# Kernel optimization log

Hardware: AMD Instinct MI355X
Metric: run time of the kernel (lower is better)

The kernel has to match this reference:

```python
import jax, jax.numpy as jnp
import numpy as np

B, T, F, OUT = 32, 8192, 128, 1024

def setup_inputs() -> dict:
    key = jax.random.key(0)
    kx, kl = jax.random.split(key)
    x = jax.random.normal(kx, (B, T, F), dtype=jnp.float32)
    # true (unpadded) lengths; module assumes max(lengths) == T (padded length)
    lengths = jax.random.randint(kl, (B,), OUT + 1, T + 1)
    lengths = lengths.at[0].set(T)
    return {"x": x, "lengths": lengths, "output_size": OUT}

def reference(x, lengths, output_size):
    # Original math: per-sample box filter of length f_b = lengths_b - output_size + 1
    # (ones / f_b, zero-padded to max) applied as grouped conv over time:
    #   out[b, t, f] = (1/f_b) * sum_{k=0}^{f_b-1} x[b, t+k, f],  t in [0, output_size)
    # Implemented via prefix sums instead of materializing the sparse filter bank.
    fsize = lengths - output_size + 1                                  # [B]
    cs = jnp.cumsum(x, axis=1)                                         # [B, T, F]
    cs = jnp.concatenate([jnp.zeros_like(cs[:, :1]), cs], axis=1)      # [B, T+1, F]
    t = jnp.arange(output_size)                                        # [OUT]
    idx = (t[None, :] + fsize[:, None])[:, :, None]                    # [B, OUT, 1]
    hi = jnp.take_along_axis(cs, idx, axis=1)                          # [B, OUT, F]
    lo = cs[:, :output_size, :]                                        # [B, OUT, F]
    return (hi - lo) / fsize[:, None, None].astype(x.dtype)
```

## Files before the change

### kernel.cpp

```cpp
#include <hip/hip_runtime.h>

#define NB   32
#define NT   8192
#define NF   128
#define NOUT 1024
#define SEGSZ 128
#define NSEG  64
#define NCHUNK 8

__device__ __forceinline__ float4 f4add(float4 a, float4 b) {
  return make_float4(a.x + b.x, a.y + b.y, a.z + b.z, a.w + b.w);
}
__device__ __forceinline__ float4 f4sub(float4 a, float4 b) {
  return make_float4(a.x - b.x, a.y - b.y, a.z - b.z, a.w - b.w);
}

__global__ __launch_bounds__(256) void seg_sums(const float* __restrict__ x,
                                                const int* __restrict__ lengths,
                                                float* __restrict__ S) {
  const int blk = blockIdx.x;
  const int b   = blk >> 6;
  const int seg = blk & (NSEG - 1);
  const int len = lengths[b];
  if (seg * SEGSZ >= len) return;

  const int tid = threadIdx.x;
  const int f4  = tid & 31;
  const int tl  = tid >> 5;

  const float4* xp =
      reinterpret_cast<const float4*>(x + (size_t)b * NT * NF +
                                      (size_t)(seg * SEGSZ) * NF) + f4;
  float4 acc = make_float4(0.f, 0.f, 0.f, 0.f);
  #pragma unroll 4
  for (int r = tl; r < SEGSZ; r += 8)
    acc = f4add(acc, xp[r * 32]);

  __shared__ float4 red[8][32];
  red[tl][f4] = acc;
  __syncthreads();
  if (tl == 0) {
    float4 s = red[0][f4];
    #pragma unroll
    for (int k = 1; k < 8; ++k) s = f4add(s, red[k][f4]);
    reinterpret_cast<float4*>(S + ((size_t)b * NSEG + seg) * NF)[f4] = s;
  }
}

__global__ __launch_bounds__(256) void window_avg(const float* __restrict__ x,
                                                  const int* __restrict__ lengths,
                                                  const float* __restrict__ S,
                                                  float* __restrict__ out) {
  const int blk = blockIdx.x;
  const int b   = blk >> 3;
  const int tc  = blk & (NCHUNK - 1);
  const int len = lengths[b];
  const int W   = len - NOUT + 1;
  const int t0  = tc * 128;
  const int p1  = t0 + W;
  const int s_hi = p1 >> 7;

  const int tid = threadIdx.x;
  const int f4  = tid & 31;
  const int tl  = tid >> 5;

  const float4* xb =
      reinterpret_cast<const float4*>(x + (size_t)b * NT * NF) + f4;
  const float4* Sb =
      reinterpret_cast<const float4*>(S + (size_t)b * NSEG * NF) + f4;

  float4 acc = make_float4(0.f, 0.f, 0.f, 0.f);
  for (int s = tc + tl; s < s_hi; s += 8)
    acc = f4add(acc, Sb[s * 32]);
  for (int j = (s_hi << 7) + tl; j < p1; j += 8)
    acc = f4add(acc, xb[j * 32]);

  __shared__ float4 red[8][32];
  red[tl][f4] = acc;
  __syncthreads();
  float4 A = make_float4(0.f, 0.f, 0.f, 0.f);
  #pragma unroll
  for (int k = 0; k < 8; ++k) A = f4add(A, red[k][f4]);
  __syncthreads();

  float4 D = make_float4(0.f, 0.f, 0.f, 0.f);
  if (tl < 7) {
    const int baseLo = t0 + 16 * tl;
    const int baseHi = p1 + 16 * tl;
    #pragma unroll 4
    for (int j = 0; j < 16; ++j) {
      float4 h = xb[(baseHi + j) * 32];
      float4 l = xb[(baseLo + j) * 32];
      D = f4add(D, f4sub(h, l));
    }
  }
  red[tl][f4] = D;
  __syncthreads();
  #pragma unroll
  for (int k = 0; k < 7; ++k)
    if (k < tl) A = f4add(A, red[k][f4]);

  const float invW = 1.0f / (float)W;
  const int tbase = t0 + 16 * tl;
  float4* ob = reinterpret_cast<float4*>(out + ((size_t)b * NOUT + tbase) * NF) + f4;

  #pragma unroll
  for (int i = 0; i < 16; ++i) {
    ob[i * 32] = make_float4(A.x * invW, A.y * invW, A.z * invW, A.w * invW);
    if (i < 15) {
      float4 h = xb[(tbase + i + W) * 32];
      float4 l = xb[(tbase + i) * 32];
      A = f4add(A, f4sub(h, l));
    }
  }
}

extern "C" void kernel_launch(void* const* d_in, const int* in_sizes, int n_in,
                              void* d_out, int out_size, void* d_ws, size_t ws_size,
                              hipStream_t stream) {
  const float* x       = (const float*)d_in[0];
  const int*   lengths = (const int*)d_in[1];
  float*       S       = (float*)d_ws;
  float*       out     = (float*)d_out;

  hipLaunchKernelGGL(seg_sums, dim3(NB * NSEG), dim3(256), 0, stream,
                     x, lengths, S);
  hipLaunchKernelGGL(window_avg, dim3(NB * NCHUNK), dim3(256), 0, stream,
                     x, lengths, S, out);
}
```

Before: 31.61 us.

## Use finer 32-row segments and tiles to quadruple window_avg block count

Segment sums are now produced at 32-row granularity (four per 128-row block), and the windowed-average kernel processes 32 output rows per block instead of 128. This gives 1024 blocks instead of 256 for the second kernel, which uses the GPU better, and shortens each thread's serial sliding-window chain. Block indices are swizzled so consecutive blocks land on different batches or XCDs. The cost is more segment sums to read per block and more redundant prefix work across tiles.

```diff
diff --git a/kernel.cpp b/kernel.cpp
--- a/kernel.cpp
+++ b/kernel.cpp
@@ -1,12 +1,13 @@
 #include <hip/hip_runtime.h>
 
-#define NB   32
-#define NT   8192
-#define NF   128
-#define NOUT 1024
-#define SEGSZ 128
-#define NSEG  64
-#define NCHUNK 8
+#define NB    32
+#define NT    8192
+#define NF    128
+#define NOUT  1024
+#define SEGSZ 32
+#define NSEG  256
+#define TILE  32
+#define NTILE (NOUT/TILE)
 
 __device__ __forceinline__ float4 f4add(float4 a, float4 b) {
   return make_float4(a.x + b.x, a.y + b.y, a.z + b.z, a.w + b.w);
@@ -20,9 +21,9 @@
                                                 float* __restrict__ S) {
   const int blk = blockIdx.x;
   const int b   = blk >> 6;
-  const int seg = blk & (NSEG - 1);
+  const int g   = blk & 63;
   const int len = lengths[b];
-  if (seg * SEGSZ >= len) return;
+  if (g * 128 >= len) return;
 
   const int tid = threadIdx.x;
   const int f4  = tid & 31;
@@ -30,20 +31,18 @@
 
   const float4* xp =
       reinterpret_cast<const float4*>(x + (size_t)b * NT * NF +
-                                      (size_t)(seg * SEGSZ) * NF) + f4;
+                                      (size_t)(g * 128) * NF) + f4;
   float4 acc = make_float4(0.f, 0.f, 0.f, 0.f);
-  #pragma unroll 4
-  for (int r = tl; r < SEGSZ; r += 8)
-    acc = f4add(acc, xp[r * 32]);
+  #pragma unroll
+  for (int r = 0; r < 16; ++r)
+    acc = f4add(acc, xp[(tl * 16 + r) * 32]);
 
   __shared__ float4 red[8][32];
   red[tl][f4] = acc;
   __syncthreads();
-  if (tl == 0) {
-    float4 s = red[0][f4];
-    #pragma unroll
-    for (int k = 1; k < 8; ++k) s = f4add(s, red[k][f4]);
-    reinterpret_cast<float4*>(S + ((size_t)b * NSEG + seg) * NF)[f4] = s;
+  if (tl < 4) {
+    float4 s = f4add(red[2 * tl][f4], red[2 * tl + 1][f4]);
+    reinterpret_cast<float4*>(S + ((size_t)b * NSEG + g * 4 + tl) * NF)[f4] = s;
   }
 }
 
@@ -51,14 +50,14 @@
                                                   const int* __restrict__ lengths,
                                                   const float* __restrict__ S,
                                                   float* __restrict__ out) {
-  const int blk = blockIdx.x;
-  const int b   = blk >> 3;
-  const int tc  = blk & (NCHUNK - 1);
-  const int len = lengths[b];
-  const int W   = len - NOUT + 1;
-  const int t0  = tc * 128;
-  const int p1  = t0 + W;
-  const int s_hi = p1 >> 7;
+  const int wg   = ((blockIdx.x & 7) << 7) + (blockIdx.x >> 3);
+  const int b    = wg >> 5;
+  const int tile = wg & (NTILE - 1);
+  const int len  = lengths[b];
+  const int W    = len - NOUT + 1;
+  const int t0   = tile * TILE;
+  const int p1   = t0 + W;
+  const int s_hi = p1 >> 5;
 
   const int tid = threadIdx.x;
   const int f4  = tid & 31;
@@ -70,9 +69,9 @@
       reinterpret_cast<const float4*>(S + (size_t)b * NSEG * NF) + f4;
 
   float4 acc = make_float4(0.f, 0.f, 0.f, 0.f);
-  for (int s = tc + tl; s < s_hi; s += 8)
+  for (int s = tile + tl; s < s_hi; s += 8)
     acc = f4add(acc, Sb[s * 32]);
-  for (int j = (s_hi << 7) + tl; j < p1; j += 8)
+  for (int j = (s_hi << 5) + tl; j < p1; j += 8)
     acc = f4add(acc, xb[j * 32]);
 
   __shared__ float4 red[8][32];
@@ -85,10 +84,10 @@
 
   float4 D = make_float4(0.f, 0.f, 0.f, 0.f);
   if (tl < 7) {
-    const int baseLo = t0 + 16 * tl;
-    const int baseHi = p1 + 16 * tl;
-    #pragma unroll 4
-    for (int j = 0; j < 16; ++j) {
+    const int baseLo = t0 + 4 * tl;
+    const int baseHi = p1 + 4 * tl;
+    #pragma unroll
+    for (int j = 0; j < 4; ++j) {
       float4 h = xb[(baseHi + j) * 32];
       float4 l = xb[(baseLo + j) * 32];
       D = f4add(D, f4sub(h, l));
@@ -100,14 +99,15 @@
   for (int k = 0; k < 7; ++k)
     if (k < tl) A = f4add(A, red[k][f4]);
 
-  const float invW = 1.0f / (float)W;
-  const int tbase = t0 + 16 * tl;
-  float4* ob = reinterpret_cast<float4*>(out + ((size_t)b * NOUT + tbase) * NF) + f4;
+  const float invW  = 1.0f / (float)W;
+  const int   tbase = t0 + 4 * tl;
+  float4* ob =
+      reinterpret_cast<float4*>(out + ((size_t)b * NOUT + tbase) * NF) + f4;
 
   #pragma unroll
-  for (int i = 0; i < 16; ++i) {
+  for (int i = 0; i < 4; ++i) {
     ob[i * 32] = make_float4(A.x * invW, A.y * invW, A.z * invW, A.w * invW);
-    if (i < 15) {
+    if (i < 3) {
       float4 h = xb[(tbase + i + W) * 32];
       float4 l = xb[(tbase + i) * 32];
       A = f4add(A, f4sub(h, l));
@@ -123,8 +123,8 @@
   float*       S       = (float*)d_ws;
   float*       out     = (float*)d_out;
 
-  hipLaunchKernelGGL(seg_sums, dim3(NB * NSEG), dim3(256), 0, stream,
+  hipLaunchKernelGGL(seg_sums, dim3(NB * 64), dim3(256), 0, stream,
                      x, lengths, S);
-  hipLaunchKernelGGL(window_avg, dim3(NB * NCHUNK), dim3(256), 0, stream,
+  hipLaunchKernelGGL(window_avg, dim3(NB * NTILE), dim3(256), 0, stream,
                      x, lengths, S, out);
 }
```

New measurement: 32.05 us. No clear change (+1.4%).
